# Kernel optimization log

Hardware: AMD Instinct MI355X
Metric: run time of the kernel (lower is better)

## Reference

```python
import jax, jax.numpy as jnp
import numpy as np
from jax import lax

D_CONV = 4


def setup_inputs() -> dict:
    key = jax.random.key(0)
    ks = jax.random.split(key, 8)
    b, L, d_model = 2, 1024, 1024
    d_inner, d_state = 2048, 16
    s = 0.02  # weight scale
    return {
        "x": jax.random.normal(ks[0], (b, L, d_model), jnp.float32),
        "in_w": jax.random.normal(ks[1], (2 * d_inner, d_model), jnp.float32) * s,
        "in_b": jnp.zeros((2 * d_inner,), jnp.float32),
        "conv_w": jax.random.normal(ks[2], (d_inner, 1, D_CONV), jnp.float32) * s,
        "conv_b": jnp.zeros((d_inner,), jnp.float32),
        "xproj_w": jax.random.normal(ks[3], (2 * d_state + 1, d_inner), jnp.float32) * s,
        "dt_w": jax.random.normal(ks[4], (d_inner, 1), jnp.float32) * s,
        "dt_b": jnp.zeros((d_inner,), jnp.float32),
        "A_log": jax.random.normal(ks[5], (d_inner, d_state), jnp.float32),
        "D": jnp.ones((d_inner,), jnp.float32),
        "out_w": jax.random.normal(ks[6], (d_model, d_inner), jnp.float32) * s,
    }


def reference(x, in_w, in_b, conv_w, conv_b, xproj_w, dt_w, dt_b, A_log, D, out_w):
    b, L, _ = x.shape
    d_inner = conv_w.shape[0]
    d_state = A_log.shape[1]

    xz = x @ in_w.T + in_b                       # (b, L, 2*d_inner)
    xh, z = jnp.split(xz, 2, axis=-1)            # each (b, L, d_inner)

    # depthwise causal conv1d (torch pads d_conv-1 both sides then slices [:L])
    xc = jnp.transpose(xh, (0, 2, 1))            # (b, d_inner, L)
    xc = lax.conv_general_dilated(
        xc, conv_w, window_strides=(1,), padding=[(D_CONV - 1, 0)],
        feature_group_count=d_inner, dimension_numbers=("NCH", "OIH", "NCH"))
    xc = xc + conv_b[None, :, None]
    xh = jnp.transpose(xc, (0, 2, 1))            # (b, L, d_inner)

    xh = xh * jax.nn.silu(z)

    proj = xh @ xproj_w.T                        # (b, L, 2*d_state+1)
    dlt = proj[..., :1]                          # (b, L, 1)
    B = proj[..., 1:1 + d_state]                 # (b, L, d_state)
    C = proj[..., 1 + d_state:]                  # (b, L, d_state)

    # dt_proj: (b,L,1) -> (b,L,d_inner); source applies softplus then exp
    delta = jnp.exp(jax.nn.softplus(dlt @ dt_w.T + dt_b))  # (b, L, d_inner)

    A = -jnp.exp(A_log)                          # (d_inner, d_state)

    def step(h, inp):
        xt, dt, Bt, Ct = inp                     # (b,i), (b,i), (b,s), (b,s)
        A_bar = jnp.exp(A[None] * dt[..., None])          # (b, i, s)
        B_bar = dt[..., None] * Bt[:, None, :]            # (b, i, s)
        h = A_bar * h + B_bar * xt[..., None]             # (b, i, s)
        yt = jnp.einsum("bis,bs->bi", h, Ct)              # (b, i)
        return h, yt

    h0 = jnp.zeros((b, d_inner, d_state), x.dtype)
    xs = (jnp.moveaxis(xh, 1, 0), jnp.moveaxis(delta, 1, 0),
          jnp.moveaxis(B, 1, 0), jnp.moveaxis(C, 1, 0))
    _, ys = lax.scan(step, h0, xs)               # (L, b, d_inner)
    y = jnp.moveaxis(ys, 0, 1) + D * xh          # (b, L, d_inner)

    return y @ out_w.T                           # (b, L, d_model)
```

## Files before the change

kernel.cpp:

```cpp
#include <hip/hip_runtime.h>
#include <hip/hip_bf16.h>

#define NTOK   2048
#define DMODEL 1024
#define DINNER 2048
#define DSTATE 16
#define SEQLEN 1024
#define NPROJ  33
#define NPAD   48
#define CCH    64
#define CT     16

typedef __attribute__((ext_vector_type(8))) short bf16x8;
typedef __attribute__((ext_vector_type(4))) float f32x4;
typedef __attribute__((ext_vector_type(8))) unsigned short us8;

__device__ __forceinline__ unsigned short f2bf(float f) {
  unsigned u = __float_as_uint(f);
  return (unsigned short)((u + 0x7FFFu + ((u >> 16) & 1u)) >> 16);
}

__device__ __forceinline__ void gload_lds16(const void* g, void* l) {
  __builtin_amdgcn_global_load_lds(
      (const __attribute__((address_space(1))) unsigned int*)g,
      (__attribute__((address_space(3))) unsigned int*)l, 16, 0, 0);
}

#define CAST_N0 (NTOK * DMODEL)
#define CAST_N1 (CAST_N0 + 2 * DINNER * DMODEL)
#define CAST_N2 (CAST_N1 + NPAD * DINNER)
__global__ __launch_bounds__(256) void cast3_bf16_kernel(
    const float* __restrict__ s0, const float* __restrict__ s1,
    const float* __restrict__ s3, unsigned short* __restrict__ dst,
    float* __restrict__ proj) {
  if (blockIdx.x < 33) {
    const int o = blockIdx.x * 2048 + threadIdx.x * 8;
    const float4 z4 = make_float4(0.f, 0.f, 0.f, 0.f);
    *(float4*)(proj + o) = z4;
    *(float4*)(proj + o + 4) = z4;
  }
  const int idx = (blockIdx.x * 256 + threadIdx.x) * 8;
  const float* src;
  int off;
  if (idx < CAST_N0) { src = s0; off = idx; }
  else if (idx < CAST_N1) { src = s1; off = idx - CAST_N0; }
  else {
    off = idx - CAST_N1;
    if (off >= NPROJ * DINNER) {
      us8 z = {0, 0, 0, 0, 0, 0, 0, 0};
      *(us8*)(dst + idx) = z;
      return;
    }
    src = s3;
  }
  const float4 a = *(const float4*)(src + off);
  const float4 b = *(const float4*)(src + off + 4);
  us8 o;
  o[0] = f2bf(a.x); o[1] = f2bf(a.y); o[2] = f2bf(a.z); o[3] = f2bf(a.w);
  o[4] = f2bf(b.x); o[5] = f2bf(b.y); o[6] = f2bf(b.z); o[7] = f2bf(b.w);
  *(us8*)(dst + idx) = o;
}

__global__ __launch_bounds__(256) void gemm_bt_mfma(
    const unsigned short* __restrict__ A, const unsigned short* __restrict__ B,
    const float* __restrict__ bias, float* __restrict__ C, int M, int K) {
  constexpr int BN = 64, TN = 2;
  __shared__ unsigned short As[2][128 * 32];
  __shared__ unsigned short Bs[2][BN * 32];

  const int tid = threadIdx.x;
  const int wid = tid >> 6;
  const int lane = tid & 63;
  const int n0 = blockIdx.x * 128;
  const int m0 = blockIdx.y * BN;

  const int wave_m = wid & 1;
  const int wave_n = wid >> 1;
  const int lm = lane & 15;
  const int lq = lane >> 4;

  f32x4 acc[4][TN] = {};

  for (int k0 = 0; k0 < K; k0 += 64) {
    __syncthreads();
#pragma unroll
    for (int h = 0; h < 2; ++h) {
      const int kh = k0 + h * 32;
#pragma unroll
      for (int j = 0; j < 2; ++j) {
        const int cb = j * 256 + wid * 64;
        const int c = cb + lane;
        gload_lds16(A + (size_t)(n0 + (c >> 2)) * K + kh + (c & 3) * 8,
                    &As[h][cb * 8]);
      }
      {
        const int cb = wid * 64;
        const int c = cb + lane;
        gload_lds16(B + (size_t)(m0 + (c >> 2)) * K + kh + (c & 3) * 8,
                    &Bs[h][cb * 8]);
      }
    }
    __syncthreads();

#pragma unroll
    for (int h = 0; h < 2; ++h) {
      bf16x8 af[4], bfr[TN];
#pragma unroll
      for (int tm = 0; tm < 4; ++tm)
        af[tm] = *(const bf16x8*)
            &As[h][(wave_m * 64 + tm * 16 + lm) * 32 + lq * 8];
#pragma unroll
      for (int tn = 0; tn < TN; ++tn)
        bfr[tn] = *(const bf16x8*)
            &Bs[h][(wave_n * (BN / 2) + tn * 16 + lm) * 32 + lq * 8];
#pragma unroll
      for (int tm = 0; tm < 4; ++tm)
#pragma unroll
        for (int tn = 0; tn < TN; ++tn)
          acc[tm][tn] = __builtin_amdgcn_mfma_f32_16x16x32_bf16(
              af[tm], bfr[tn], acc[tm][tn], 0, 0, 0);
    }
  }

#pragma unroll
  for (int tm = 0; tm < 4; ++tm) {
    const int row = n0 + wave_m * 64 + tm * 16 + lq * 4;
#pragma unroll
    for (int tn = 0; tn < TN; ++tn) {
      const int col = m0 + wave_n * (BN / 2) + tn * 16 + lm;
      const float bv = bias[col];
#pragma unroll
      for (int r = 0; r < 4; ++r)
        C[(size_t)(row + r) * M + col] = acc[tm][tn][r] + bv;
    }
  }
}

__global__ __launch_bounds__(256) void gemm_bt_mfma_sk(
    const unsigned short* __restrict__ A, const unsigned short* __restrict__ B,
    float* __restrict__ C, int M, int K) {
  constexpr int BN = 64, TN = 2;
  __shared__ unsigned short As[2][128 * 32];
  __shared__ unsigned short Bs[2][BN * 32];

  const int tid = threadIdx.x;
  const int wid = tid >> 6;
  const int lane = tid & 63;
  const int n0 = blockIdx.x * 128;
  const int m0 = blockIdx.y * BN;
  const int kstart = blockIdx.z * (K >> 2);

  const int wave_m = wid & 1;
  const int wave_n = wid >> 1;
  const int lm = lane & 15;
  const int lq = lane >> 4;

  f32x4 acc[4][TN] = {};

  for (int k0 = kstart; k0 < kstart + (K >> 2); k0 += 64) {
    __syncthreads();
#pragma unroll
    for (int h = 0; h < 2; ++h) {
      const int kh = k0 + h * 32;
#pragma unroll
      for (int j = 0; j < 2; ++j) {
        const int cb = j * 256 + wid * 64;
        const int c = cb + lane;
        gload_lds16(A + (size_t)(n0 + (c >> 2)) * K + kh + (c & 3) * 8,
                    &As[h][cb * 8]);
      }
      {
        const int cb = wid * 64;
        const int c = cb + lane;
        gload_lds16(B + (size_t)(m0 + (c >> 2)) * K + kh + (c & 3) * 8,
                    &Bs[h][cb * 8]);
      }
    }
    __syncthreads();

#pragma unroll
    for (int h = 0; h < 2; ++h) {
      bf16x8 af[4], bfr[TN];
#pragma unroll
      for (int tm = 0; tm < 4; ++tm)
        af[tm] = *(const bf16x8*)
            &As[h][(wave_m * 64 + tm * 16 + lm) * 32 + lq * 8];
#pragma unroll
      for (int tn = 0; tn < TN; ++tn)
        bfr[tn] = *(const bf16x8*)
            &Bs[h][(wave_n * (BN / 2) + tn * 16 + lm) * 32 + lq * 8];
#pragma unroll
      for (int tm = 0; tm < 4; ++tm)
#pragma unroll
        for (int tn = 0; tn < TN; ++tn)
          acc[tm][tn] = __builtin_amdgcn_mfma_f32_16x16x32_bf16(
              af[tm], bfr[tn], acc[tm][tn], 0, 0, 0);
    }
  }

#pragma unroll
  for (int tm = 0; tm < 4; ++tm) {
    const int row = n0 + wave_m * 64 + tm * 16 + lq * 4;
#pragma unroll
    for (int tn = 0; tn < TN; ++tn) {
      const int col = m0 + wave_n * (BN / 2) + tn * 16 + lm;
#pragma unroll
      for (int r = 0; r < 4; ++r)
        atomicAdd(&C[(size_t)(row + r) * M + col], acc[tm][tn][r]);
    }
  }
}

__global__ __launch_bounds__(256) void conv_xproj_mfma(
    const float* __restrict__ xz, const float* __restrict__ cw,
    const float* __restrict__ cb, const unsigned short* __restrict__ wp,
    float* __restrict__ xg, float* __restrict__ proj) {
  __shared__ unsigned short As[4][64 * 32];
  __shared__ unsigned short Bs[4][NPAD * 32];

  const int tid = threadIdx.x;
  const int wid = tid >> 6;
  const int lane = tid & 63;
  const int n0 = blockIdx.x * 64;
  const int kb = blockIdx.y * 128;

#pragma unroll
  for (int j = 0; j < 3; ++j) {
    const int cbase = j * 256 + wid * 64;
    const int c = cbase + lane;
    const int stage = c / 192;
    const int rem = c - stage * 192;
    gload_lds16(wp + (size_t)(rem >> 2) * DINNER + kb + stage * 32 + (rem & 3) * 8,
                &Bs[0][0] + cbase * 8);
  }

  const int c128 = tid & 127;
  const int half = tid >> 7;
  const int i = kb + c128;
  const int gt0 = n0 + half * 32;
  const float4 w4 = ((const float4*)cw)[i];
  const float cbv = cb[i];

  const bool seq_start = ((gt0 & (SEQLEN - 1)) == 0);
  float tm3 = seq_start ? 0.f : xz[(size_t)(gt0 - 3) * (2 * DINNER) + i];
  float tm2 = seq_start ? 0.f : xz[(size_t)(gt0 - 2) * (2 * DINNER) + i];
  float tm1 = seq_start ? 0.f : xz[(size_t)(gt0 - 1) * (2 * DINNER) + i];

  unsigned short* Arow = &As[c128 >> 5][c128 & 31];
#pragma unroll 4
  for (int t = 0; t < 32; ++t) {
    const int n = gt0 + t;
    const float x0 = xz[(size_t)n * (2 * DINNER) + i];
    float acc = cbv;
    acc = fmaf(w4.x, tm3, acc);
    acc = fmaf(w4.y, tm2, acc);
    acc = fmaf(w4.z, tm1, acc);
    acc = fmaf(w4.w, x0, acc);
    const float z = xz[(size_t)n * (2 * DINNER) + DINNER + i];
    const float sig = 1.f / (1.f + __expf(-z));
    const float v = acc * (z * sig);
    xg[(size_t)n * DINNER + i] = v;
    Arow[(half * 32 + t) * 32] = f2bf(v);
    tm3 = tm2; tm2 = tm1; tm1 = x0;
  }
  __syncthreads();

  const int lm = lane & 15;
  const int lq = lane >> 4;
  f32x4 acc[3] = {};
#pragma unroll
  for (int stage = 0; stage < 4; ++stage) {
    bf16x8 af = *(const bf16x8*)&As[stage][(wid * 16 + lm) * 32 + lq * 8];
#pragma unroll
    for (int tn = 0; tn < 3; ++tn) {
      bf16x8 bfr = *(const bf16x8*)&Bs[stage][(tn * 16 + lm) * 32 + lq * 8];
      acc[tn] = __builtin_amdgcn_mfma_f32_16x16x32_bf16(af, bfr, acc[tn], 0, 0, 0);
    }
  }

  const int row = n0 + wid * 16 + lq * 4;
#pragma unroll
  for (int tn = 0; tn < 3; ++tn) {
    const int col = tn * 16 + lm;
    if (col < NPROJ) {
#pragma unroll
      for (int r = 0; r < 4; ++r)
        atomicAdd(&proj[(size_t)(row + r) * NPROJ + col], acc[tn][r]);
    }
  }
}

__global__ __launch_bounds__(256) void scan_phase1(
    const float* __restrict__ xg, const float* __restrict__ proj,
    const float* __restrict__ dt_w, const float* __restrict__ dt_b,
    const float* __restrict__ A_log,
    float* __restrict__ Sbuf, float* __restrict__ Hbuf) {
  __shared__ float pl[CT][36];
  const int tid = threadIdx.x;
  const int i = blockIdx.x * 256 + tid;
  const int k = blockIdx.y;
  const int b = blockIdx.z;
  const int n0 = b * SEQLEN + k * CT;

  for (int e = tid; e < CT * NPROJ; e += 256) {
    const int t = e / NPROJ;
    const int c = e - t * NPROJ;
    pl[t][c] = proj[(size_t)(n0 + t) * NPROJ + c];
  }
  __syncthreads();

  const float dtw = dt_w[i], dtb = dt_b[i];
  float Av[DSTATE];
#pragma unroll
  for (int s = 0; s < DSTATE; ++s) Av[s] = -__expf(A_log[i * DSTATE + s]);

  float h[DSTATE] = {};
  float Ssum = 0.f;

  for (int t = 0; t < CT; ++t) {
    const float delta = 1.f + __expf(fmaf(pl[t][0], dtw, dtb));
    Ssum += delta;
    const float x = xg[(size_t)(n0 + t) * DINNER + i];
    const float dx = delta * x;
#pragma unroll
    for (int s = 0; s < DSTATE; ++s)
      h[s] = fmaf(__expf(Av[s] * delta), h[s], pl[t][1 + s] * dx);
  }

  const size_t ck = (size_t)(b * CCH + k) * DINNER + i;
  Sbuf[ck] = Ssum;
  float4* Hq = (float4*)(Hbuf + ck * DSTATE);
#pragma unroll
  for (int q = 0; q < 4; ++q)
    Hq[q] = make_float4(h[4 * q], h[4 * q + 1], h[4 * q + 2], h[4 * q + 3]);
}

__global__ __launch_bounds__(256) void scan_phase2(
    const float* __restrict__ A_log, const float* __restrict__ Sbuf,
    float* __restrict__ Hbuf, float* __restrict__ out,
    const float* __restrict__ out_w, unsigned short* __restrict__ outw_bf) {
  const int gid = blockIdx.x * 256 + threadIdx.x;
  const float4 z4 = make_float4(0.f, 0.f, 0.f, 0.f);
#pragma unroll
  for (int j = 0; j < 8; ++j)
    *(float4*)(out + (size_t)(j * 65536 + gid) * 4) = z4;

  {
    const int base = gid * 32;
#pragma unroll
    for (int q = 0; q < 4; ++q) {
      const float4 a = *(const float4*)(out_w + base + q * 8);
      const float4 b = *(const float4*)(out_w + base + q * 8 + 4);
      us8 o;
      o[0] = f2bf(a.x); o[1] = f2bf(a.y); o[2] = f2bf(a.z); o[3] = f2bf(a.w);
      o[4] = f2bf(b.x); o[5] = f2bf(b.y); o[6] = f2bf(b.z); o[7] = f2bf(b.w);
      *(us8*)(outw_bf + base + q * 8) = o;
    }
  }

  const int s = gid & (DSTATE - 1);
  const int i = (gid >> 4) & (DINNER - 1);
  const int b = gid >> 15;
  const float Av = -__expf(A_log[i * DSTATE + s]);
  float H = 0.f;
  for (int k = 0; k < CCH; ++k) {
    const size_t ck = (size_t)(b * CCH + k) * DINNER + i;
    const float hk = Hbuf[ck * DSTATE + s];
    const float a = __expf(Av * Sbuf[ck]);
    Hbuf[ck * DSTATE + s] = H;
    H = fmaf(a, H, hk);
  }
}

__global__ __launch_bounds__(256) void scan_phase3(
    const float* __restrict__ xg, const float* __restrict__ proj,
    const float* __restrict__ dt_w, const float* __restrict__ dt_b,
    const float* __restrict__ A_log, const float* __restrict__ Dp,
    const float* __restrict__ Hbuf, unsigned short* __restrict__ y) {
  __shared__ float pl[CT][36];
  const int tid = threadIdx.x;
  const int i = blockIdx.x * 256 + tid;
  const int k = blockIdx.y;
  const int b = blockIdx.z;
  const int n0 = b * SEQLEN + k * CT;

  for (int e = tid; e < CT * NPROJ; e += 256) {
    const int t = e / NPROJ;
    const int c = e - t * NPROJ;
    pl[t][c] = proj[(size_t)(n0 + t) * NPROJ + c];
  }
  __syncthreads();

  const float dtw = dt_w[i], dtb = dt_b[i];
  const float Dv = Dp[i];
  float Av[DSTATE];
#pragma unroll
  for (int s = 0; s < DSTATE; ++s) Av[s] = -__expf(A_log[i * DSTATE + s]);

  const size_t ck = (size_t)(b * CCH + k) * DINNER + i;
  float h[DSTATE];
  const float4* Hq = (const float4*)(Hbuf + ck * DSTATE);
#pragma unroll
  for (int q = 0; q < 4; ++q) {
    const float4 v = Hq[q];
    h[4 * q + 0] = v.x; h[4 * q + 1] = v.y;
    h[4 * q + 2] = v.z; h[4 * q + 3] = v.w;
  }

  for (int t = 0; t < CT; ++t) {
    const float delta = 1.f + __expf(fmaf(pl[t][0], dtw, dtb));
    const float x = xg[(size_t)(n0 + t) * DINNER + i];
    const float dx = delta * x;
    float yt = 0.f;
#pragma unroll
    for (int s = 0; s < DSTATE; ++s) {
      h[s] = fmaf(__expf(Av[s] * delta), h[s], pl[t][1 + s] * dx);
      yt = fmaf(h[s], pl[t][17 + s], yt);
    }
    y[(size_t)(n0 + t) * DINNER + i] = f2bf(fmaf(Dv, x, yt));
  }
}

extern "C" void kernel_launch(void* const* d_in, const int* in_sizes, int n_in,
                              void* d_out, int out_size, void* d_ws, size_t ws_size,
                              hipStream_t stream) {
  const float* x       = (const float*)d_in[0];
  const float* in_w    = (const float*)d_in[1];
  const float* in_b    = (const float*)d_in[2];
  const float* conv_w  = (const float*)d_in[3];
  const float* conv_b  = (const float*)d_in[4];
  const float* xproj_w = (const float*)d_in[5];
  const float* dt_w    = (const float*)d_in[6];
  const float* dt_b    = (const float*)d_in[7];
  const float* A_log   = (const float*)d_in[8];
  const float* Dp      = (const float*)d_in[9];
  const float* out_w   = (const float*)d_in[10];
  float* out = (float*)d_out;

  float* ws = (float*)d_ws;
  float* xz = ws;
  float* xg = ws + 8388608;
  unsigned short* bf_base = (unsigned short*)(ws + 12582912);
  unsigned short* x_bf    = bf_base;
  unsigned short* inw_bf  = bf_base + CAST_N0;
  unsigned short* wpad_bf = bf_base + CAST_N1;
  unsigned short* outw_bf = bf_base + CAST_N2;
  unsigned short* yb_bf = (unsigned short*)(ws + 16826368);
  float* proj = ws + 18923520;
  float* Sbuf = ws + 19005440;
  float* Hbuf = ws + 19267584;

  cast3_bf16_kernel<<<CAST_N2 / (256 * 8), 256, 0, stream>>>(
      x, in_w, xproj_w, bf_base, proj);

  gemm_bt_mfma<<<dim3(NTOK / 128, (2 * DINNER) / 64), 256, 0, stream>>>(
      x_bf, inw_bf, in_b, xz, 2 * DINNER, DMODEL);

  conv_xproj_mfma<<<dim3(NTOK / 64, DINNER / 128), 256, 0, stream>>>(
      xz, conv_w, conv_b, wpad_bf, xg, proj);

  scan_phase1<<<dim3(DINNER / 256, CCH, 2), 256, 0, stream>>>(
      xg, proj, dt_w, dt_b, A_log, Sbuf, Hbuf);
  scan_phase2<<<(2 * DINNER * DSTATE) / 256, 256, 0, stream>>>(
      A_log, Sbuf, Hbuf, out, out_w, outw_bf);
  scan_phase3<<<dim3(DINNER / 256, CCH, 2), 256, 0, stream>>>(
      xg, proj, dt_w, dt_b, A_log, Dp, Hbuf, yb_bf);

  gemm_bt_mfma_sk<<<dim3(NTOK / 128, DMODEL / 64, 4), 256, 0, stream>>>(
      yb_bf, outw_bf, out, DMODEL, DINNER);
}
```

Baseline: 225.5 us.

## Store in-proj output as bf16, widen its tile, halve out-proj split-K

```diff
diff --git a/kernel.cpp b/kernel.cpp
--- a/kernel.cpp
+++ b/kernel.cpp
@@ -18,6 +18,9 @@
 __device__ __forceinline__ unsigned short f2bf(float f) {
   unsigned u = __float_as_uint(f);
   return (unsigned short)((u + 0x7FFFu + ((u >> 16) & 1u)) >> 16);
+}
+__device__ __forceinline__ float bf2f(unsigned short u) {
+  return __uint_as_float(((unsigned)u) << 16);
 }
 
 __device__ __forceinline__ void gload_lds16(const void* g, void* l) {
@@ -63,8 +66,9 @@
 
 __global__ __launch_bounds__(256) void gemm_bt_mfma(
     const unsigned short* __restrict__ A, const unsigned short* __restrict__ B,
-    const float* __restrict__ bias, float* __restrict__ C, int M, int K) {
-  constexpr int BN = 64, TN = 2;
+    const float* __restrict__ bias, unsigned short* __restrict__ C,
+    int M, int K) {
+  constexpr int BN = 128, TN = 4;
   __shared__ unsigned short As[2][128 * 32];
   __shared__ unsigned short Bs[2][BN * 32];
 
@@ -82,6 +86,83 @@
   f32x4 acc[4][TN] = {};
 
   for (int k0 = 0; k0 < K; k0 += 64) {
+    __syncthreads();
+#pragma unroll
+    for (int h = 0; h < 2; ++h) {
+      const int kh = k0 + h * 32;
+#pragma unroll
+      for (int j = 0; j < 2; ++j) {
+        const int cb = j * 256 + wid * 64;
+        const int c = cb + lane;
+        gload_lds16(A + (size_t)(n0 + (c >> 2)) * K + kh + (c & 3) * 8,
+                    &As[h][cb * 8]);
+      }
+#pragma unroll
+      for (int j = 0; j < BN / 64; ++j) {
+        const int cb = j * 256 + wid * 64;
+        const int c = cb + lane;
+        gload_lds16(B + (size_t)(m0 + (c >> 2)) * K + kh + (c & 3) * 8,
+                    &Bs[h][cb * 8]);
+      }
+    }
+    __syncthreads();
+
+#pragma unroll
+    for (int h = 0; h < 2; ++h) {
+      bf16x8 af[4], bfr[TN];
+#pragma unroll
+      for (int tm = 0; tm < 4; ++tm)
+        af[tm] = *(const bf16x8*)
+            &As[h][(wave_m * 64 + tm * 16 + lm) * 32 + lq * 8];
+#pragma unroll
+      for (int tn = 0; tn < TN; ++tn)
+        bfr[tn] = *(const bf16x8*)
+            &Bs[h][(wave_n * (BN / 2) + tn * 16 + lm) * 32 + lq * 8];
+#pragma unroll
+      for (int tm = 0; tm < 4; ++tm)
+#pragma unroll
+        for (int tn = 0; tn < TN; ++tn)
+          acc[tm][tn] = __builtin_amdgcn_mfma_f32_16x16x32_bf16(
+              af[tm], bfr[tn], acc[tm][tn], 0, 0, 0);
+    }
+  }
+
+#pragma unroll
+  for (int tm = 0; tm < 4; ++tm) {
+    const int row = n0 + wave_m * 64 + tm * 16 + lq * 4;
+#pragma unroll
+    for (int tn = 0; tn < TN; ++tn) {
+      const int col = m0 + wave_n * (BN / 2) + tn * 16 + lm;
+      const float bv = bias[col];
+#pragma unroll
+      for (int r = 0; r < 4; ++r)
+        C[(size_t)(row + r) * M + col] = f2bf(acc[tm][tn][r] + bv);
+    }
+  }
+}
+
+__global__ __launch_bounds__(256) void gemm_bt_mfma_sk(
+    const unsigned short* __restrict__ A, const unsigned short* __restrict__ B,
+    float* __restrict__ C, int M, int K) {
+  constexpr int BN = 64, TN = 2;
+  __shared__ unsigned short As[2][128 * 32];
+  __shared__ unsigned short Bs[2][BN * 32];
+
+  const int tid = threadIdx.x;
+  const int wid = tid >> 6;
+  const int lane = tid & 63;
+  const int n0 = blockIdx.x * 128;
+  const int m0 = blockIdx.y * BN;
+  const int kstart = blockIdx.z * (K >> 1);
+
+  const int wave_m = wid & 1;
+  const int wave_n = wid >> 1;
+  const int lm = lane & 15;
+  const int lq = lane >> 4;
+
+  f32x4 acc[4][TN] = {};
+
+  for (int k0 = kstart; k0 < kstart + (K >> 1); k0 += 64) {
     __syncthreads();
 #pragma unroll
     for (int h = 0; h < 2; ++h) {
@@ -128,82 +209,6 @@
 #pragma unroll
     for (int tn = 0; tn < TN; ++tn) {
       const int col = m0 + wave_n * (BN / 2) + tn * 16 + lm;
-      const float bv = bias[col];
-#pragma unroll
-      for (int r = 0; r < 4; ++r)
-        C[(size_t)(row + r) * M + col] = acc[tm][tn][r] + bv;
-    }
-  }
-}
-
-__global__ __launch_bounds__(256) void gemm_bt_mfma_sk(
-    const unsigned short* __restrict__ A, const unsigned short* __restrict__ B,
-    float* __restrict__ C, int M, int K) {
-  constexpr int BN = 64, TN = 2;
-  __shared__ unsigned short As[2][128 * 32];
-  __shared__ unsigned short Bs[2][BN * 32];
-
-  const int tid = threadIdx.x;
-  const int wid = tid >> 6;
-  const int lane = tid & 63;
-  const int n0 = blockIdx.x * 128;
-  const int m0 = blockIdx.y * BN;
-  const int kstart = blockIdx.z * (K >> 2);
-
-  const int wave_m = wid & 1;
-  const int wave_n = wid >> 1;
-  const int lm = lane & 15;
-  const int lq = lane >> 4;
-
-  f32x4 acc[4][TN] = {};
-
-  for (int k0 = kstart; k0 < kstart + (K >> 2); k0 += 64) {
-    __syncthreads();
-#pragma unroll
-    for (int h = 0; h < 2; ++h) {
-      const int kh = k0 + h * 32;
-#pragma unroll
-      for (int j = 0; j < 2; ++j) {
-        const int cb = j * 256 + wid * 64;
-        const int c = cb + lane;
-        gload_lds16(A + (size_t)(n0 + (c >> 2)) * K + kh + (c & 3) * 8,
-                    &As[h][cb * 8]);
-      }
-      {
-        const int cb = wid * 64;
-        const int c = cb + lane;
-        gload_lds16(B + (size_t)(m0 + (c >> 2)) * K + kh + (c & 3) * 8,
-                    &Bs[h][cb * 8]);
-      }
-    }
-    __syncthreads();
-
-#pragma unroll
-    for (int h = 0; h < 2; ++h) {
-      bf16x8 af[4], bfr[TN];
-#pragma unroll
-      for (int tm = 0; tm < 4; ++tm)
-        af[tm] = *(const bf16x8*)
-            &As[h][(wave_m * 64 + tm * 16 + lm) * 32 + lq * 8];
-#pragma unroll
-      for (int tn = 0; tn < TN; ++tn)
-        bfr[tn] = *(const bf16x8*)
-            &Bs[h][(wave_n * (BN / 2) + tn * 16 + lm) * 32 + lq * 8];
-#pragma unroll
-      for (int tm = 0; tm < 4; ++tm)
-#pragma unroll
-        for (int tn = 0; tn < TN; ++tn)
-          acc[tm][tn] = __builtin_amdgcn_mfma_f32_16x16x32_bf16(
-              af[tm], bfr[tn], acc[tm][tn], 0, 0, 0);
-    }
-  }
-
-#pragma unroll
-  for (int tm = 0; tm < 4; ++tm) {
-    const int row = n0 + wave_m * 64 + tm * 16 + lq * 4;
-#pragma unroll
-    for (int tn = 0; tn < TN; ++tn) {
-      const int col = m0 + wave_n * (BN / 2) + tn * 16 + lm;
 #pragma unroll
       for (int r = 0; r < 4; ++r)
         atomicAdd(&C[(size_t)(row + r) * M + col], acc[tm][tn][r]);
@@ -212,7 +217,7 @@
 }
 
 __global__ __launch_bounds__(256) void conv_xproj_mfma(
-    const float* __restrict__ xz, const float* __restrict__ cw,
+    const unsigned short* __restrict__ xz, const float* __restrict__ cw,
     const float* __restrict__ cb, const unsigned short* __restrict__ wp,
     float* __restrict__ xg, float* __restrict__ proj) {
   __shared__ unsigned short As[4][64 * 32];
@@ -242,21 +247,21 @@
   const float cbv = cb[i];
 
   const bool seq_start = ((gt0 & (SEQLEN - 1)) == 0);
-  float tm3 = seq_start ? 0.f : xz[(size_t)(gt0 - 3) * (2 * DINNER) + i];
-  float tm2 = seq_start ? 0.f : xz[(size_t)(gt0 - 2) * (2 * DINNER) + i];
-  float tm1 = seq_start ? 0.f : xz[(size_t)(gt0 - 1) * (2 * DINNER) + i];
+  float tm3 = seq_start ? 0.f : bf2f(xz[(size_t)(gt0 - 3) * (2 * DINNER) + i]);
+  float tm2 = seq_start ? 0.f : bf2f(xz[(size_t)(gt0 - 2) * (2 * DINNER) + i]);
+  float tm1 = seq_start ? 0.f : bf2f(xz[(size_t)(gt0 - 1) * (2 * DINNER) + i]);
 
   unsigned short* Arow = &As[c128 >> 5][c128 & 31];
 #pragma unroll 4
   for (int t = 0; t < 32; ++t) {
     const int n = gt0 + t;
-    const float x0 = xz[(size_t)n * (2 * DINNER) + i];
+    const float x0 = bf2f(xz[(size_t)n * (2 * DINNER) + i]);
     float acc = cbv;
     acc = fmaf(w4.x, tm3, acc);
     acc = fmaf(w4.y, tm2, acc);
     acc = fmaf(w4.z, tm1, acc);
     acc = fmaf(w4.w, x0, acc);
-    const float z = xz[(size_t)n * (2 * DINNER) + DINNER + i];
+    const float z = bf2f(xz[(size_t)n * (2 * DINNER) + DINNER + i]);
     const float sig = 1.f / (1.f + __expf(-z));
     const float v = acc * (z * sig);
     xg[(size_t)n * DINNER + i] = v;
@@ -438,7 +443,7 @@
   float* out = (float*)d_out;
 
   float* ws = (float*)d_ws;
-  float* xz = ws;
+  unsigned short* xz_bf = (unsigned short*)ws;
   float* xg = ws + 8388608;
   unsigned short* bf_base = (unsigned short*)(ws + 12582912);
   unsigned short* x_bf    = bf_base;
@@ -453,11 +458,11 @@
   cast3_bf16_kernel<<<CAST_N2 / (256 * 8), 256, 0, stream>>>(
       x, in_w, xproj_w, bf_base, proj);
 
-  gemm_bt_mfma<<<dim3(NTOK / 128, (2 * DINNER) / 64), 256, 0, stream>>>(
-      x_bf, inw_bf, in_b, xz, 2 * DINNER, DMODEL);
+  gemm_bt_mfma<<<dim3(NTOK / 128, (2 * DINNER) / 128), 256, 0, stream>>>(
+      x_bf, inw_bf, in_b, xz_bf, 2 * DINNER, DMODEL);
 
   conv_xproj_mfma<<<dim3(NTOK / 64, DINNER / 128), 256, 0, stream>>>(
-      xz, conv_w, conv_b, wpad_bf, xg, proj);
+      xz_bf, conv_w, conv_b, wpad_bf, xg, proj);
 
   scan_phase1<<<dim3(DINNER / 256, CCH, 2), 256, 0, stream>>>(
       xg, proj, dt_w, dt_b, A_log, Sbuf, Hbuf);
@@ -466,6 +471,6 @@
   scan_phase3<<<dim3(DINNER / 256, CCH, 2), 256, 0, stream>>>(
       xg, proj, dt_w, dt_b, A_log, Dp, Hbuf, yb_bf);
 
-  gemm_bt_mfma_sk<<<dim3(NTOK / 128, DMODEL / 64, 4), 256, 0, stream>>>(
+  gemm_bt_mfma_sk<<<dim3(NTOK / 128, DMODEL / 64, 2), 256, 0, stream>>>(
       yb_bf, outw_bf, out, DMODEL, DINNER);
 }
```

Measured after the change: 213.5 us. -5.3%, faster.
